# Kernel optimization log

Hardware: AMD Instinct MI355X
Metric: run time of the kernel (lower is better)

The kernel has to match this reference:

```python
import math
import jax, jax.numpy as jnp
import numpy as np

C = 64
GRID = 2

def _conv1x1(x, W, b):
    # 1x1 conv == channel-mixing matmul: [B,C,H,W] x [O,C] -> [B,O,H,W]
    return jnp.einsum('bchw,oc->bohw', x, W) + b[None, :, None, None]

def setup_inputs() -> dict:
    key = jax.random.key(0)
    ks = jax.random.split(key, 11)
    s = 1.0 / math.sqrt(C)
    def w(k):
        return jax.random.normal(k, (C, C), dtype=jnp.float32) * s
    def bias(k):
        return jax.random.normal(k, (C,), dtype=jnp.float32) * 0.02
    return {
        'x': jax.random.normal(ks[0], (2, C, 128, 128), dtype=jnp.float32),
        'Wq': w(ks[1]), 'bq': bias(ks[2]),
        'Wk': w(ks[3]), 'bk': bias(ks[4]),
        'Wa': w(ks[5]), 'ba': bias(ks[6]),
        'Wb': w(ks[7]), 'bb': bias(ks[8]),
        'Wo': w(ks[9]), 'bo': bias(ks[10]),
    }

def reference(x, Wq, bq, Wk, bk, Wa, ba, Wb, bb, Wo, bo):
    B, c, H, W = x.shape
    g = GRID
    rh, rw = H // g, W // g  # H,W chosen divisible by grid -> no reflect pad
    N = rh * rw
    R = g * g

    q = _conv1x1(x, Wq, bq)
    k = _conv1x1(x, Wk, bk)
    a = _conv1x1(x, Wa, ba)
    bt = _conv1x1(x, Wb, bb)

    def regionize(t):
        # [B,C,H,W] -> [B, R, C, N] with N = rh*rw row-major per region
        return t.reshape(B, c, g, rh, g, rw).transpose(0, 2, 4, 1, 3, 5).reshape(B, R, c, N)

    qr, kr, ar, br = regionize(q), regionize(k), regionize(a), regionize(bt)

    # attn[b,r,n,m] = softmax_m( q^T k / sqrt(C) )
    attn = jax.nn.softmax(jnp.einsum('brcn,brcm->brnm', qr, kr) / math.sqrt(c), axis=-1)

    # out_r = alpha @ attn + beta @ attn^T
    out = (jnp.einsum('brcj,brjm->brcm', ar, attn)
           + jnp.einsum('brcj,brmj->brcm', br, attn))

    # [B,R,C,N] -> [B,C,H,W]
    out = out.reshape(B, g, g, c, rh, rw).transpose(0, 3, 1, 4, 2, 5).reshape(B, c, H, W)
    return _conv1x1(out, Wo, bo)
```

## Files before the change

kernel.cpp:

```cpp
#include <hip/hip_runtime.h>


typedef __attribute__((ext_vector_type(8)))  short bf16x8;
typedef __attribute__((ext_vector_type(16))) float f32x16;

#define MFMA32(a, b, c) __builtin_amdgcn_mfma_f32_32x32x16_bf16(a, b, c, 0, 0, 0)

constexpr int REG_ELEMS = 4096 * 64;
constexpr size_t QP_OFF    = 0;
constexpr size_t KP_OFF    = 4u  << 20;
constexpr size_t ATL_OFF   = 8u  << 20;
constexpr size_t BTL_OFF   = 12u << 20;
constexpr size_t P0_OFF    = 16u << 20;
constexpr size_t P1_OFF    = 24u << 20;
constexpr size_t LNV_OFF   = 32u << 20;
constexpr size_t LPART_OFF = (32u << 20) + (128u << 10);

constexpr float QSCALE = 0.18033688011112042f;

__device__ __forceinline__ short f2bf(float f) {
    union { float f; unsigned u; } v; v.f = f;
    unsigned r = v.u + 0x7fffu + ((v.u >> 16) & 1u);
    return (short)(r >> 16);
}
__device__ __forceinline__ float bf2f(short s) {
    union { unsigned u; float f; } v; v.u = ((unsigned)(unsigned short)s) << 16;
    return v.f;
}
__device__ __forceinline__ unsigned fbits(float f) {
    union { float f; unsigned u; } v; v.f = f; return v.u;
}
__device__ __forceinline__ unsigned pack_trunc(float e0, float e1) {
    return __builtin_amdgcn_perm(fbits(e1), fbits(e0), 0x07060302u);
}
__device__ __forceinline__ f32x16 zero16() {
    f32x16 z;
    #pragma unroll
    for (int i = 0; i < 16; ++i) z[i] = 0.f;
    return z;
}
__device__ __forceinline__ float fexp2(float x) {
#if __has_builtin(__builtin_amdgcn_exp2f)
    return __builtin_amdgcn_exp2f(x);
#else
    return exp2f(x);
#endif
}
__device__ __forceinline__ void permswap32(unsigned& a, unsigned& b, bool hi) {
#if __has_builtin(__builtin_amdgcn_permlane32_swap)
    auto r = __builtin_amdgcn_permlane32_swap(a, b, false, false);
    a = r[0]; b = r[1];
#elif __has_builtin(__builtin_amdgcn_permlane32_swap_b32)
    auto r = __builtin_amdgcn_permlane32_swap_b32(a, b, false, false);
    a = r[0]; b = r[1];
#else
    unsigned ax = (unsigned)__shfl_xor((int)a, 32);
    unsigned bx = (unsigned)__shfl_xor((int)b, 32);
    unsigned na = hi ? bx : a;
    unsigned nb = hi ? b  : ax;
    a = na; b = nb;
#endif
}

typedef __attribute__((address_space(1))) const unsigned char as1_t;
typedef __attribute__((address_space(3))) unsigned char as3_t;
__device__ __forceinline__ void stage16(const void* g, void* l) {
    __builtin_amdgcn_global_load_lds((as1_t*)g, (as3_t*)l, 16, 0, 0);
}

__global__ __launch_bounds__(256) void k_conv_in(
    const float* __restrict__ x,
    const float* __restrict__ Wq, const float* __restrict__ bq,
    const float* __restrict__ Wk, const float* __restrict__ bk,
    const float* __restrict__ Wa, const float* __restrict__ ba,
    const float* __restrict__ Wb, const float* __restrict__ bb,
    char* __restrict__ ws)
{
    const int tid  = threadIdx.x;
    const int blk  = blockIdx.x;
    const int wseg = blk & 1;
    const int h    = (blk >> 1) & 127;
    const int b    = blk >> 8;
    const int br   = b * 4 + (h >> 6) * 2 + wseg;
    const int n0   = (h & 63) * 64;

    __shared__ float xs[64][68];
    __shared__ short trans[2][64][72];

    const float* xp = x + ((size_t)b * 64 * 16384) + (size_t)h * 128 + wseg * 64;
    #pragma unroll
    for (int r = 0; r < 4; ++r) {
        int idx = r * 256 + tid;
        int c   = idx >> 4;
        int w4  = (idx & 15) << 2;
        *(float4*)&xs[c][w4] = *(const float4*)(xp + (size_t)c * 16384 + w4);
    }
    __syncthreads();

    const int lane = tid & 63;
    const int wid  = tid >> 6;
    const int col  = lane & 31;
    const int l5   = lane >> 5;
    const int pH   = wid & 1;
    const int oH   = wid >> 1;
    const int px   = pH * 32 + col;
    const int oc   = oH * 32 + col;

    bf16x8 xhi[4], xlo[4];
    #pragma unroll
    for (int s = 0; s < 4; ++s) {
        union { bf16x8 v; short sh[8]; } uh, ul;
        #pragma unroll
        for (int e = 0; e < 8; ++e) {
            float xv = xs[s * 16 + l5 * 8 + e][px];
            short hh = f2bf(xv);
            uh.sh[e] = hh;
            ul.sh[e] = f2bf(xv - bf2f(hh));
        }
        xhi[s] = uh.v; xlo[s] = ul.v;
    }

    #pragma unroll
    for (int mat = 0; mat < 4; ++mat) {
        const float* Wsel = (mat == 0) ? Wq : (mat == 1) ? Wk : (mat == 2) ? Wa : Wb;
        const float* bsel = (mat == 0) ? bq : (mat == 1) ? bk : (mat == 2) ? ba : bb;

        bf16x8 whi[4], wlo[4];
        const float* wrow = Wsel + (size_t)oc * 64;
        #pragma unroll
        for (int s = 0; s < 4; ++s) {
            float4 f0 = *(const float4*)(wrow + s * 16 + l5 * 8);
            float4 f1 = *(const float4*)(wrow + s * 16 + l5 * 8 + 4);
            float wf[8] = { f0.x, f0.y, f0.z, f0.w, f1.x, f1.y, f1.z, f1.w };
            union { bf16x8 v; short sh[8]; } uh, ul;
            #pragma unroll
            for (int e = 0; e < 8; ++e) {
                short hh = f2bf(wf[e]);
                uh.sh[e] = hh;
                ul.sh[e] = f2bf(wf[e] - bf2f(hh));
            }
            whi[s] = uh.v; wlo[s] = ul.v;
        }

        f32x16 d = zero16();
        #pragma unroll
        for (int s = 0; s < 4; ++s) {
            d = MFMA32(xhi[s], whi[s], d);
            d = MFMA32(xhi[s], wlo[s], d);
            d = MFMA32(xlo[s], whi[s], d);
        }

        const float bias = bsel[oc];
        if (mat < 2) {
            const float sc = (mat == 0) ? QSCALE : 1.0f;
            #pragma unroll
            for (int r = 0; r < 16; ++r) {
                int pxl = pH * 32 + (r & 3) + 8 * (r >> 2) + 4 * l5;
                trans[mat][pxl][oc] = f2bf((d[r] + bias) * sc);
            }
        } else {
            short* base = (short*)(ws + (mat == 2 ? ATL_OFF : BTL_OFF))
                          + (size_t)br * REG_ELEMS;
            const int sw   = (oc >> 1) & 3;
            const int tile = (n0 >> 5) + pH;
            #pragma unroll
            for (int q = 0; q < 4; ++q) {
                short tmp4[4];
                #pragma unroll
                for (int rr = 0; rr < 4; ++rr) tmp4[rr] = f2bf(d[4 * q + rr] + bias);
                int segp = q ^ sw;
                short* p = base + (size_t)tile * 2048 + oc * 32 + segp * 8 + 4 * l5;
                *(uint2*)p = *(uint2*)tmp4;
            }
        }
    }
    __syncthreads();

    #pragma unroll
    for (int rep = 0; rep < 4; ++rep) {
        int idx  = rep * 256 + tid;
        int mat2 = idx >> 9;
        int row  = (idx >> 3) & 63;
        int seg  = idx & 7;
        short* dst = (short*)(ws + (mat2 ? KP_OFF : QP_OFF))
                     + (size_t)br * REG_ELEMS + (size_t)(n0 + row) * 64
                     + (seg ^ (row & 7)) * 8;
        *(uint4*)dst = *(uint4*)&trans[mat2][row][seg * 8];
    }
}

__global__ __launch_bounds__(256, 2) void k_stats(char* __restrict__ ws)
{
    const int tid  = threadIdx.x;
    const int br   = blockIdx.x & 7;
    const int nt   = (blockIdx.x >> 3) & 63;
    const int ms   = blockIdx.x >> 9;
    const int lane = tid & 63;
    const int w    = tid >> 6;
    const int wn   = w & 1;
    const int wi   = w >> 1;
    const int col  = lane & 31;
    const int l5   = lane >> 5;

    const short* Qb  = (const short*)(ws + QP_OFF) + (size_t)br * REG_ELEMS;
    const char*  Kbb = ws + KP_OFF + (size_t)br * REG_ELEMS * 2
                       + (size_t)ms * 262144;

    __shared__ __align__(16) char smem[16896];

    const int nrow = nt * 64 + wn * 32 + col;
    bf16x8 afr[4];
    #pragma unroll
    for (int s = 0; s < 4; ++s)
        afr[s] = *(const bf16x8*)(Qb + (size_t)nrow * 64 + (((2*s+l5) ^ (col & 7)) * 8));

    float sm[16];
    #pragma unroll
    for (int r = 0; r < 16; ++r) sm[r] = 0.f;

    {
        const char* g = Kbb + (size_t)w * 2048 + lane * 16;
        char* l = smem + w * 2048;
        stage16(g, l); stage16(g + 1024, l + 1024);
    }

    #pragma unroll 2
    for (int slab = 0; slab < 32; ++slab) {
        __syncthreads();
        if (slab + 1 < 32) {
            const char* g = Kbb + (size_t)(slab + 1) * 8192 + w * 2048 + lane * 16;
            char* l = smem + ((slab + 1) & 1) * 8192 + w * 2048;
            stage16(g, l); stage16(g + 1024, l + 1024);
        }
        const short* Ks = (const short*)(smem + (slab & 1) * 8192);
        f32x16 d = zero16();
        #pragma unroll
        for (int s = 0; s < 4; ++s) {
            bf16x8 bf = *(const bf16x8*)(Ks + (wi * 32 + col) * 64
                                         + ((2*s+l5) ^ (col & 7)) * 8);
            d = MFMA32(afr[s], bf, d);
        }
        #pragma unroll
        for (int r = 0; r < 16; ++r) sm[r] += fexp2(d[r]);
    }

    #pragma unroll
    for (int off = 1; off < 32; off <<= 1)
        #pragma unroll
        for (int r = 0; r < 16; ++r) sm[r] += __shfl_xor(sm[r], off);

    __syncthreads();
    float* Lred = (float*)(smem + 16384);
    if (col == 0) {
        #pragma unroll
        for (int r = 0; r < 16; ++r)
            Lred[w * 32 + ((r & 3) + 8 * (r >> 2) + 4 * l5)] = sm[r];
    }
    __syncthreads();
    if (tid < 64) {
        int wn2 = tid >> 5, nl = tid & 31;
        float L = Lred[wn2 * 32 + nl] + Lred[(wn2 + 2) * 32 + nl];
        ((float*)(ws + LPART_OFF))[(size_t)ms * 32768 + (size_t)br * 4096
                                   + nt * 64 + tid] = L;
    }
}

__global__ __launch_bounds__(256) void k_ascale(char* __restrict__ ws)
{
    const int tid = threadIdx.x;
    const int br  = blockIdx.x & 7;
    const int nt  = blockIdx.x >> 3;

    __shared__ float Larr[64];

    if (tid < 64) {
        const float* Lp = (const float*)(ws + LPART_OFF);
        const size_t idx = (size_t)br * 4096 + nt * 64 + tid;
        float li = 1.0f / (Lp[idx] + Lp[32768 + idx]);
        Larr[tid] = li;
        ((float*)(ws + LNV_OFF))[idx] = li;
    }
    __syncthreads();

    short* Ab = (short*)(ws + ATL_OFF) + (size_t)br * REG_ELEMS + (size_t)nt * 4096;
    #pragma unroll
    for (int rep = 0; rep < 2; ++rep) {
        int id = rep * 256 + tid;
        int t = id >> 8, c = (id >> 2) & 63, s = id & 3;
        int sg = s ^ ((c >> 1) & 3);
        int jl = t * 32 + sg * 8;
        short* p = Ab + (size_t)t * 2048 + c * 32 + s * 8;
        uint4 v = *(uint4*)p;
        short* sp = (short*)&v;
        short o[8];
        #pragma unroll
        for (int e = 0; e < 8; ++e) o[e] = f2bf(bf2f(sp[e]) * Larr[jl + e]);
        *(uint4*)p = *(uint4*)o;
    }
}

__global__ __launch_bounds__(512, 2) void k_attn(char* __restrict__ ws)
{
    const int tid  = threadIdx.x;
    const int br   = blockIdx.x & 7;
    const int mt   = (blockIdx.x >> 3) & 31;
    const int js   = blockIdx.x >> 8;
    const int lane = tid & 63;
    const int w    = tid >> 6;
    const int wj   = w & 1;
    const int jsw  = (w >> 1) & 1;
    const int mh   = w >> 2;
    const int col  = lane & 31;
    const int l5   = lane >> 5;
    const bool hi  = (l5 != 0);

    const char* Qbb = ws + QP_OFF  + (size_t)br * REG_ELEMS * 2;
    const char* Kbb = ws + KP_OFF  + (size_t)br * REG_ELEMS * 2;
    const char* Abb = ws + ATL_OFF + (size_t)br * REG_ELEMS * 2;
    const char* Bbb = ws + BTL_OFF + (size_t)br * REG_ELEMS * 2;
    const float* Lnv = (const float*)(ws + LNV_OFF) + (size_t)br * 4096;
    float* Pp = (float*)(ws + (js ? P1_OFF : P0_OFF)) + (size_t)br * REG_ELEMS;

    __shared__ __align__(16) char smem[65536];

    const short* msrcb = (const short*)(wj == 0 ? Kbb : Qbb);
    bf16x8 mf[2][4];
    #pragma unroll
    for (int h = 0; h < 2; ++h) {
        const short* mr = msrcb + (size_t)(mt * 128 + mh * 64 + h * 32 + col) * 64;
        #pragma unroll
        for (int s = 0; s < 4; ++s)
            mf[h][s] = *(const bf16x8*)(mr + ((2*s+l5) ^ (col & 7)) * 8);
    }

    f32x16 acc00 = zero16(), acc01 = zero16();
    f32x16 acc10 = zero16(), acc11 = zero16();

    const int tt = w & 3;
    const int hh = w >> 2;
    const char* gsb = (tt == 0) ? Qbb : (tt == 1) ? Kbb : (tt == 2) ? Abb : Bbb;

    {
        const char* g = gsb + (size_t)hh * 262144 + (size_t)js * 131072 + lane * 16;
        char* l = smem + hh * 16384 + tt * 4096 + lane * 16;
        #pragma unroll
        for (int i = 0; i < 4; ++i) stage16(g + i * 1024, l + i * 1024);
    }

    #pragma unroll 2
    for (int rnd = 0; rnd < 32; ++rnd) {
        __syncthreads();
        if (rnd + 1 < 32) {
            const char* g = gsb + (size_t)hh * 262144 + (size_t)js * 131072
                            + (size_t)(rnd + 1) * 4096 + lane * 16;
            char* l = smem + ((rnd + 1) & 1) * 32768 + hh * 16384
                      + tt * 4096 + lane * 16;
            #pragma unroll
            for (int i = 0; i < 4; ++i) stage16(g + i * 1024, l + i * 1024);
        }
        const char* sb = smem + (rnd & 1) * 32768 + jsw * 16384;
        const short* jr = (const short*)(sb + (wj == 0 ? 0 : 4096));
        const short* ts = (const short*)(sb + (wj == 0 ? 8192 : 12288));

        bf16x8 a[4];
        #pragma unroll
        for (int s = 0; s < 4; ++s)
            a[s] = *(const bf16x8*)(jr + col * 64 + ((2*s+l5) ^ (col & 7)) * 8);

        f32x16 d0 = zero16(), d1 = zero16();
        #pragma unroll
        for (int s = 0; s < 4; ++s) {
            d0 = MFMA32(a[s], mf[0][s], d0);
            d1 = MFMA32(a[s], mf[1][s], d1);
        }

        unsigned W0[8], W1[8];
        #pragma unroll
        for (int q = 0; q < 4; ++q) {
            W0[2*q]   = pack_trunc(fexp2(d0[4*q]),   fexp2(d0[4*q+1]));
            W0[2*q+1] = pack_trunc(fexp2(d0[4*q+2]), fexp2(d0[4*q+3]));
            W1[2*q]   = pack_trunc(fexp2(d1[4*q]),   fexp2(d1[4*q+1]));
            W1[2*q+1] = pack_trunc(fexp2(d1[4*q+2]), fexp2(d1[4*q+3]));
        }

        #pragma unroll
        for (int k16 = 0; k16 < 2; ++k16) {
            unsigned u0 = W0[4*k16+0], u1 = W0[4*k16+1];
            unsigned u2 = W0[4*k16+2], u3 = W0[4*k16+3];
            permswap32(u0, u2, hi);
            permswap32(u1, u3, hi);
            union { uint4 u; bf16x8 v; } fr0;
            fr0.u.x = u0; fr0.u.y = u1; fr0.u.z = u2; fr0.u.w = u3;

            unsigned v0 = W1[4*k16+0], v1 = W1[4*k16+1];
            unsigned v2 = W1[4*k16+2], v3 = W1[4*k16+3];
            permswap32(v0, v2, hi);
            permswap32(v1, v3, hi);
            union { uint4 u; bf16x8 v; } fr1;
            fr1.u.x = v0; fr1.u.y = v1; fr1.u.z = v2; fr1.u.w = v3;

            const int swz = ((2*k16 + l5) ^ ((col >> 1) & 3)) * 8;
            bf16x8 bL = *(const bf16x8*)(ts + col * 32 + swz);
            bf16x8 bH = *(const bf16x8*)(ts + (col + 32) * 32 + swz);
            acc00 = MFMA32(fr0.v, bL, acc00);
            acc01 = MFMA32(fr0.v, bH, acc01);
            acc10 = MFMA32(fr1.v, bL, acc10);
            acc11 = MFMA32(fr1.v, bH, acc11);
        }
    }

    __syncthreads();
    float* red = (float*)smem;
    const int low2 = w & 3;
    if (low2 == 0) {
        #pragma unroll
        for (int h = 0; h < 2; ++h)
            #pragma unroll
            for (int r = 0; r < 16; ++r) {
                int ml = mh * 64 + h * 32 + (r & 3) + 8 * (r >> 2) + 4 * l5;
                red[ml * 68 + col]      = h ? acc10[r] : acc00[r];
                red[ml * 68 + 32 + col] = h ? acc11[r] : acc01[r];
            }
    }
    __syncthreads();
    if (low2 == 2) {
        #pragma unroll
        for (int h = 0; h < 2; ++h)
            #pragma unroll
            for (int r = 0; r < 16; ++r) {
                int ml = mh * 64 + h * 32 + (r & 3) + 8 * (r >> 2) + 4 * l5;
                red[ml * 68 + col]      += h ? acc10[r] : acc00[r];
                red[ml * 68 + 32 + col] += h ? acc11[r] : acc01[r];
            }
    }
    __syncthreads();
    if (low2 == 1) {
        #pragma unroll
        for (int h = 0; h < 2; ++h)
            #pragma unroll
            for (int r = 0; r < 16; ++r) {
                int ml = mh * 64 + h * 32 + (r & 3) + 8 * (r >> 2) + 4 * l5;
                float li = Lnv[mt * 128 + ml];
                red[ml * 68 + col]      += li * (h ? acc10[r] : acc00[r]);
                red[ml * 68 + 32 + col] += li * (h ? acc11[r] : acc01[r]);
            }
    }
    __syncthreads();
    if (low2 == 3) {
        #pragma unroll
        for (int h = 0; h < 2; ++h)
            #pragma unroll
            for (int r = 0; r < 16; ++r) {
                int ml = mh * 64 + h * 32 + (r & 3) + 8 * (r >> 2) + 4 * l5;
                float li = Lnv[mt * 128 + ml];
                red[ml * 68 + col]      += li * (h ? acc10[r] : acc00[r]);
                red[ml * 68 + 32 + col] += li * (h ? acc11[r] : acc01[r]);
            }
    }
    __syncthreads();
    {
        const int m  = tid >> 2;
        const int c0 = (tid & 3) * 16;
        const float* rp = red + m * 68 + c0;
        float* orow = Pp + (size_t)(mt * 128 + m) * 64 + c0;
        #pragma unroll
        for (int i = 0; i < 4; ++i)
            *(float4*)(orow + i * 4) = *(const float4*)(rp + i * 4);
    }
}

__global__ __launch_bounds__(256) void k_conv_out(
    const char* __restrict__ ws,
    const float* __restrict__ Wo, const float* __restrict__ bo,
    float* __restrict__ out)
{
    const int tid  = threadIdx.x;
    const int lane = tid & 63;
    const int sub  = tid >> 6;
    const int blk  = blockIdx.x;
    const int br   = blk & 7;
    const int nt   = (blk >> 3) * 4 + sub;
    const int col  = lane & 31;
    const int l5   = lane >> 5;

    const float* Pa = (const float*)(ws + P0_OFF) + (size_t)br * REG_ELEMS;
    const float* Pb = (const float*)(ws + P1_OFF) + (size_t)br * REG_ELEMS;

    bf16x8 afr[4];
    const size_t roff = (size_t)(nt * 32 + col) * 64 + l5 * 8;
    #pragma unroll
    for (int s = 0; s < 4; ++s) {
        float4 a0 = *(const float4*)(Pa + roff + s * 16);
        float4 a1 = *(const float4*)(Pa + roff + s * 16 + 4);
        float4 b0 = *(const float4*)(Pb + roff + s * 16);
        float4 b1 = *(const float4*)(Pb + roff + s * 16 + 4);
        union { bf16x8 v; short sh[8]; } u;
        u.sh[0] = f2bf(a0.x + b0.x); u.sh[1] = f2bf(a0.y + b0.y);
        u.sh[2] = f2bf(a0.z + b0.z); u.sh[3] = f2bf(a0.w + b0.w);
        u.sh[4] = f2bf(a1.x + b1.x); u.sh[5] = f2bf(a1.y + b1.y);
        u.sh[6] = f2bf(a1.z + b1.z); u.sh[7] = f2bf(a1.w + b1.w);
        afr[s] = u.v;
    }

    bf16x8 bw[2][4];
    #pragma unroll
    for (int oh = 0; oh < 2; ++oh) {
        const float* wrow = Wo + (size_t)(oh * 32 + col) * 64 + l5 * 8;
        #pragma unroll
        for (int s = 0; s < 4; ++s) {
            float4 f0 = *(const float4*)(wrow + s * 16);
            float4 f1 = *(const float4*)(wrow + s * 16 + 4);
            union { bf16x8 v; short sh[8]; } u;
            u.sh[0] = f2bf(f0.x); u.sh[1] = f2bf(f0.y);
            u.sh[2] = f2bf(f0.z); u.sh[3] = f2bf(f0.w);
            u.sh[4] = f2bf(f1.x); u.sh[5] = f2bf(f1.y);
            u.sh[6] = f2bf(f1.z); u.sh[7] = f2bf(f1.w);
            bw[oh][s] = u.v;
        }
    }

    f32x16 d0 = zero16(), d1 = zero16();
    #pragma unroll
    for (int s = 0; s < 4; ++s) {
        d0 = MFMA32(afr[s], bw[0][s], d0);
        d1 = MFMA32(afr[s], bw[1][s], d1);
    }

    const int b  = br >> 2;
    const int gi = (br >> 1) & 1;
    const int gj = br & 1;

    #pragma unroll
    for (int oh = 0; oh < 2; ++oh) {
        const int oc = oh * 32 + col;
        const float bias = bo[oc];
        const f32x16& d = oh ? d1 : d0;
        #pragma unroll
        for (int q = 0; q < 4; ++q) {
            int nloc = 8 * q + 4 * l5;
            int nreg = nt * 32 + nloc;
            int wp   = nreg & 63;
            int ip   = nreg >> 6;
            float4 v = make_float4(d[4*q+0] + bias, d[4*q+1] + bias,
                                   d[4*q+2] + bias, d[4*q+3] + bias);
            float* op = out + ((size_t)(b * 64 + oc)) * 16384
                        + (size_t)(gi * 64 + ip) * 128 + gj * 64 + wp;
            *(float4*)op = v;
        }
    }
}

extern "C" void kernel_launch(void* const* d_in, const int* in_sizes, int n_in,
                              void* d_out, int out_size, void* d_ws, size_t ws_size,
                              hipStream_t stream)
{
    const float* x  = (const float*)d_in[0];
    const float* Wq = (const float*)d_in[1];
    const float* bq = (const float*)d_in[2];
    const float* Wk = (const float*)d_in[3];
    const float* bk = (const float*)d_in[4];
    const float* Wa = (const float*)d_in[5];
    const float* ba = (const float*)d_in[6];
    const float* Wb = (const float*)d_in[7];
    const float* bb = (const float*)d_in[8];
    const float* Wo = (const float*)d_in[9];
    const float* bo = (const float*)d_in[10];
    char* ws   = (char*)d_ws;
    float* out = (float*)d_out;

    hipLaunchKernelGGL(k_conv_in,  dim3(512),  dim3(256), 0, stream,
                       x, Wq, bq, Wk, bk, Wa, ba, Wb, bb, ws);
    hipLaunchKernelGGL(k_stats,    dim3(1024), dim3(256), 0, stream, ws);
    hipLaunchKernelGGL(k_ascale,   dim3(512),  dim3(256), 0, stream, ws);
    hipLaunchKernelGGL(k_attn,     dim3(512),  dim3(512), 0, stream, ws);
    hipLaunchKernelGGL(k_conv_out, dim3(256),  dim3(256), 0, stream,
                       ws, Wo, bo, out);
}
```

Before: 210.0 us.

## Halve attention block size by looping over both j-slices per wave

```diff
diff --git a/kernel.cpp b/kernel.cpp
--- a/kernel.cpp
+++ b/kernel.cpp
@@ -299,7 +299,7 @@
     }
 }
 
-__global__ __launch_bounds__(512, 2) void k_attn(char* __restrict__ ws)
+__global__ __launch_bounds__(256, 2) void k_attn(char* __restrict__ ws)
 {
     const int tid  = threadIdx.x;
     const int br   = blockIdx.x & 7;
@@ -308,8 +308,7 @@
     const int lane = tid & 63;
     const int w    = tid >> 6;
     const int wj   = w & 1;
-    const int jsw  = (w >> 1) & 1;
-    const int mh   = w >> 2;
+    const int mh   = w >> 1;
     const int col  = lane & 31;
     const int l5   = lane >> 5;
     const bool hi  = (l5 != 0);
@@ -336,83 +335,92 @@
     f32x16 acc00 = zero16(), acc01 = zero16();
     f32x16 acc10 = zero16(), acc11 = zero16();
 
-    const int tt = w & 3;
-    const int hh = w >> 2;
+    const int tt = w;
     const char* gsb = (tt == 0) ? Qbb : (tt == 1) ? Kbb : (tt == 2) ? Abb : Bbb;
 
     {
-        const char* g = gsb + (size_t)hh * 262144 + (size_t)js * 131072 + lane * 16;
-        char* l = smem + hh * 16384 + tt * 4096 + lane * 16;
-        #pragma unroll
-        for (int i = 0; i < 4; ++i) stage16(g + i * 1024, l + i * 1024);
+        #pragma unroll
+        for (int hh = 0; hh < 2; ++hh) {
+            const char* g = gsb + (size_t)hh * 262144 + (size_t)js * 131072
+                            + lane * 16;
+            char* l = smem + hh * 16384 + tt * 4096 + lane * 16;
+            #pragma unroll
+            for (int i = 0; i < 4; ++i) stage16(g + i * 1024, l + i * 1024);
+        }
     }
 
     #pragma unroll 2
     for (int rnd = 0; rnd < 32; ++rnd) {
         __syncthreads();
         if (rnd + 1 < 32) {
-            const char* g = gsb + (size_t)hh * 262144 + (size_t)js * 131072
-                            + (size_t)(rnd + 1) * 4096 + lane * 16;
-            char* l = smem + ((rnd + 1) & 1) * 32768 + hh * 16384
-                      + tt * 4096 + lane * 16;
-            #pragma unroll
-            for (int i = 0; i < 4; ++i) stage16(g + i * 1024, l + i * 1024);
-        }
-        const char* sb = smem + (rnd & 1) * 32768 + jsw * 16384;
-        const short* jr = (const short*)(sb + (wj == 0 ? 0 : 4096));
-        const short* ts = (const short*)(sb + (wj == 0 ? 8192 : 12288));
-
-        bf16x8 a[4];
-        #pragma unroll
-        for (int s = 0; s < 4; ++s)
-            a[s] = *(const bf16x8*)(jr + col * 64 + ((2*s+l5) ^ (col & 7)) * 8);
-
-        f32x16 d0 = zero16(), d1 = zero16();
-        #pragma unroll
-        for (int s = 0; s < 4; ++s) {
-            d0 = MFMA32(a[s], mf[0][s], d0);
-            d1 = MFMA32(a[s], mf[1][s], d1);
-        }
-
-        unsigned W0[8], W1[8];
-        #pragma unroll
-        for (int q = 0; q < 4; ++q) {
-            W0[2*q]   = pack_trunc(fexp2(d0[4*q]),   fexp2(d0[4*q+1]));
-            W0[2*q+1] = pack_trunc(fexp2(d0[4*q+2]), fexp2(d0[4*q+3]));
-            W1[2*q]   = pack_trunc(fexp2(d1[4*q]),   fexp2(d1[4*q+1]));
-            W1[2*q+1] = pack_trunc(fexp2(d1[4*q+2]), fexp2(d1[4*q+3]));
-        }
-
-        #pragma unroll
-        for (int k16 = 0; k16 < 2; ++k16) {
-            unsigned u0 = W0[4*k16+0], u1 = W0[4*k16+1];
-            unsigned u2 = W0[4*k16+2], u3 = W0[4*k16+3];
-            permswap32(u0, u2, hi);
-            permswap32(u1, u3, hi);
-            union { uint4 u; bf16x8 v; } fr0;
-            fr0.u.x = u0; fr0.u.y = u1; fr0.u.z = u2; fr0.u.w = u3;
-
-            unsigned v0 = W1[4*k16+0], v1 = W1[4*k16+1];
-            unsigned v2 = W1[4*k16+2], v3 = W1[4*k16+3];
-            permswap32(v0, v2, hi);
-            permswap32(v1, v3, hi);
-            union { uint4 u; bf16x8 v; } fr1;
-            fr1.u.x = v0; fr1.u.y = v1; fr1.u.z = v2; fr1.u.w = v3;
-
-            const int swz = ((2*k16 + l5) ^ ((col >> 1) & 3)) * 8;
-            bf16x8 bL = *(const bf16x8*)(ts + col * 32 + swz);
-            bf16x8 bH = *(const bf16x8*)(ts + (col + 32) * 32 + swz);
-            acc00 = MFMA32(fr0.v, bL, acc00);
-            acc01 = MFMA32(fr0.v, bH, acc01);
-            acc10 = MFMA32(fr1.v, bL, acc10);
-            acc11 = MFMA32(fr1.v, bH, acc11);
+            #pragma unroll
+            for (int hh = 0; hh < 2; ++hh) {
+                const char* g = gsb + (size_t)hh * 262144 + (size_t)js * 131072
+                                + (size_t)(rnd + 1) * 4096 + lane * 16;
+                char* l = smem + ((rnd + 1) & 1) * 32768 + hh * 16384
+                          + tt * 4096 + lane * 16;
+                #pragma unroll
+                for (int i = 0; i < 4; ++i) stage16(g + i * 1024, l + i * 1024);
+            }
+        }
+
+        #pragma unroll
+        for (int jsw = 0; jsw < 2; ++jsw) {
+            const char* sb = smem + (rnd & 1) * 32768 + jsw * 16384;
+            const short* jr = (const short*)(sb + (wj == 0 ? 0 : 4096));
+            const short* ts = (const short*)(sb + (wj == 0 ? 8192 : 12288));
+
+            bf16x8 a[4];
+            #pragma unroll
+            for (int s = 0; s < 4; ++s)
+                a[s] = *(const bf16x8*)(jr + col * 64 + ((2*s+l5) ^ (col & 7)) * 8);
+
+            f32x16 d0 = zero16(), d1 = zero16();
+            #pragma unroll
+            for (int s = 0; s < 4; ++s) {
+                d0 = MFMA32(a[s], mf[0][s], d0);
+                d1 = MFMA32(a[s], mf[1][s], d1);
+            }
+
+            unsigned W0[8], W1[8];
+            #pragma unroll
+            for (int q = 0; q < 4; ++q) {
+                W0[2*q]   = pack_trunc(fexp2(d0[4*q]),   fexp2(d0[4*q+1]));
+                W0[2*q+1] = pack_trunc(fexp2(d0[4*q+2]), fexp2(d0[4*q+3]));
+                W1[2*q]   = pack_trunc(fexp2(d1[4*q]),   fexp2(d1[4*q+1]));
+                W1[2*q+1] = pack_trunc(fexp2(d1[4*q+2]), fexp2(d1[4*q+3]));
+            }
+
+            #pragma unroll
+            for (int k16 = 0; k16 < 2; ++k16) {
+                unsigned u0 = W0[4*k16+0], u1 = W0[4*k16+1];
+                unsigned u2 = W0[4*k16+2], u3 = W0[4*k16+3];
+                permswap32(u0, u2, hi);
+                permswap32(u1, u3, hi);
+                union { uint4 u; bf16x8 v; } fr0;
+                fr0.u.x = u0; fr0.u.y = u1; fr0.u.z = u2; fr0.u.w = u3;
+
+                unsigned v0 = W1[4*k16+0], v1 = W1[4*k16+1];
+                unsigned v2 = W1[4*k16+2], v3 = W1[4*k16+3];
+                permswap32(v0, v2, hi);
+                permswap32(v1, v3, hi);
+                union { uint4 u; bf16x8 v; } fr1;
+                fr1.u.x = v0; fr1.u.y = v1; fr1.u.z = v2; fr1.u.w = v3;
+
+                const int swz = ((2*k16 + l5) ^ ((col >> 1) & 3)) * 8;
+                bf16x8 bL = *(const bf16x8*)(ts + col * 32 + swz);
+                bf16x8 bH = *(const bf16x8*)(ts + (col + 32) * 32 + swz);
+                acc00 = MFMA32(fr0.v, bL, acc00);
+                acc01 = MFMA32(fr0.v, bH, acc01);
+                acc10 = MFMA32(fr1.v, bL, acc10);
+                acc11 = MFMA32(fr1.v, bH, acc11);
+            }
         }
     }
 
     __syncthreads();
     float* red = (float*)smem;
-    const int low2 = w & 3;
-    if (low2 == 0) {
+    if (wj == 0) {
         #pragma unroll
         for (int h = 0; h < 2; ++h)
             #pragma unroll
@@ -423,18 +431,7 @@
             }
     }
     __syncthreads();
-    if (low2 == 2) {
-        #pragma unroll
-        for (int h = 0; h < 2; ++h)
-            #pragma unroll
-            for (int r = 0; r < 16; ++r) {
-                int ml = mh * 64 + h * 32 + (r & 3) + 8 * (r >> 2) + 4 * l5;
-                red[ml * 68 + col]      += h ? acc10[r] : acc00[r];
-                red[ml * 68 + 32 + col] += h ? acc11[r] : acc01[r];
-            }
-    }
-    __syncthreads();
-    if (low2 == 1) {
+    if (wj == 1) {
         #pragma unroll
         for (int h = 0; h < 2; ++h)
             #pragma unroll
@@ -446,25 +443,13 @@
             }
     }
     __syncthreads();
-    if (low2 == 3) {
-        #pragma unroll
-        for (int h = 0; h < 2; ++h)
-            #pragma unroll
-            for (int r = 0; r < 16; ++r) {
-                int ml = mh * 64 + h * 32 + (r & 3) + 8 * (r >> 2) + 4 * l5;
-                float li = Lnv[mt * 128 + ml];
-                red[ml * 68 + col]      += li * (h ? acc10[r] : acc00[r]);
-                red[ml * 68 + 32 + col] += li * (h ? acc11[r] : acc01[r]);
-            }
-    }
-    __syncthreads();
     {
-        const int m  = tid >> 2;
-        const int c0 = (tid & 3) * 16;
+        const int m  = tid >> 1;
+        const int c0 = (tid & 1) * 32;
         const float* rp = red + m * 68 + c0;
         float* orow = Pp + (size_t)(mt * 128 + m) * 64 + c0;
         #pragma unroll
-        for (int i = 0; i < 4; ++i)
+        for (int i = 0; i < 8; ++i)
             *(float4*)(orow + i * 4) = *(const float4*)(rp + i * 4);
     }
 }
@@ -572,7 +557,7 @@
                        x, Wq, bq, Wk, bk, Wa, ba, Wb, bb, ws);
     hipLaunchKernelGGL(k_stats,    dim3(1024), dim3(256), 0, stream, ws);
     hipLaunchKernelGGL(k_ascale,   dim3(512),  dim3(256), 0, stream, ws);
-    hipLaunchKernelGGL(k_attn,     dim3(512),  dim3(512), 0, stream, ws);
+    hipLaunchKernelGGL(k_attn,     dim3(512),  dim3(256), 0, stream, ws);
     hipLaunchKernelGGL(k_conv_out, dim3(256),  dim3(256), 0, stream,
                        ws, Wo, bo, out);
 }
```

New measurement: 202.0 us. 1.04x faster.
